# Optimization experiments

Measured on AMD Instinct MI355X. Metric: run time of the kernel, lower is better.

Reference implementation:

```python
import jax, jax.numpy as jnp
import numpy as np


def conv2d(x, w, b):
    # x: [B, Cin, H, W], w: [Cout, Cin, 3, 3] -> SAME 3x3 conv, stride 1
    y = jax.lax.conv_general_dilated(x, w, (1, 1), 'SAME',
                                     dimension_numbers=('NCHW', 'OIHW', 'NCHW'))
    return y + b[None, :, None, None]


def trilinear_interpolation(data, offsets, sample_nums):
    """data: [B, D(frames), C, H, W]; offsets: [B, sample_nums*3, H, W]
    Returns samples [B, sample_nums, C, H, W] via trilinear interp over (d,h,w)."""
    B, D, C, H, W = data.shape
    S = sample_nums
    off = offsets.reshape(B, S, 3, H, W)
    # base 3x3x3 grid centered at middle frame / current pixel
    g = jnp.arange(S)
    kd = (g // 9 - 1).astype(jnp.float32)        # [S]
    kh = ((g // 3) % 3 - 1).astype(jnp.float32)
    kw = (g % 3 - 1).astype(jnp.float32)
    center = (D - 1) / 2.0
    hh = jnp.arange(H, dtype=jnp.float32)
    ww = jnp.arange(W, dtype=jnp.float32)
    pd = center + kd[None, :, None, None] + off[:, :, 0]                 # [B,S,H,W]
    ph = hh[None, None, :, None] + kh[None, :, None, None] + off[:, :, 1]
    pw = ww[None, None, None, :] + kw[None, :, None, None] + off[:, :, 2]
    pd = jnp.clip(pd, 0.0, D - 1.0)
    ph = jnp.clip(ph, 0.0, H - 1.0)
    pw = jnp.clip(pw, 0.0, W - 1.0)
    d0 = jnp.floor(pd); h0 = jnp.floor(ph); w0 = jnp.floor(pw)
    fd = pd - d0; fh = ph - h0; fw = pw - w0
    d0i = d0.astype(jnp.int32); h0i = h0.astype(jnp.int32); w0i = w0.astype(jnp.int32)
    d1i = jnp.minimum(d0i + 1, D - 1)
    h1i = jnp.minimum(h0i + 1, H - 1)
    w1i = jnp.minimum(w0i + 1, W - 1)
    # flatten (d,h,w) for gather, keep channels contiguous
    data_flat = data.transpose(0, 2, 1, 3, 4).reshape(B, C, D * H * W)

    def gather(di, hi, wi):
        idx = ((di * H + hi) * W + wi).reshape(B, 1, S * H * W)
        g_ = jnp.take_along_axis(data_flat, idx, axis=2)   # [B,C,S*H*W]
        return g_.reshape(B, C, S, H, W).transpose(0, 2, 1, 3, 4)  # [B,S,C,H,W]

    out = jnp.zeros((B, S, C, H, W), dtype=data.dtype)
    for di, wd in ((d0i, 1.0 - fd), (d1i, fd)):
        for hi, wh in ((h0i, 1.0 - fh), (h1i, fh)):
            for wi, wwgt in ((w0i, 1.0 - fw), (w1i, fw)):
                wgt = (wd * wh * wwgt)[:, :, None]  # [B,S,1,H,W]
                out = out + wgt * gather(di, hi, wi)
    return out


SAMPLE_NUMS = 27
GROUPS = 3


def setup_inputs() -> dict:
    key = jax.random.key(0)
    ks = jax.random.split(key, 14)
    B, BURST, C, H, W = 4, 5, 3, 256, 256
    in_len = BURST * C          # 15
    ch_w = in_len + 128 + SAMPLE_NUMS * C  # 224
    s = 0.05
    p = lambda k, sh: jax.random.normal(k, sh, dtype=jnp.float32) * s
    return {
        'data': jax.random.normal(ks[0], (B, BURST, C, H, W), dtype=jnp.float32),
        'enc_w1': p(ks[1], (64, in_len, 3, 3)), 'enc_b1': jnp.zeros((64,), jnp.float32),
        'enc_w2': p(ks[2], (128, 64, 3, 3)),    'enc_b2': jnp.zeros((128,), jnp.float32),
        'off_w':  p(ks[3], (SAMPLE_NUMS * 3, 128, 3, 3)), 'off_b': jnp.zeros((SAMPLE_NUMS * 3,), jnp.float32),
        'wc_w1':  p(ks[4], (64, ch_w, 3, 3)),   'wc_b1': jnp.zeros((64,), jnp.float32),
        'wc_w2':  p(ks[5], (64, 64, 3, 3)),     'wc_b2': jnp.zeros((64,), jnp.float32),
        'wc_w3':  p(ks[6], (SAMPLE_NUMS, 64, 3, 3)), 'wc_b3': jnp.zeros((SAMPLE_NUMS,), jnp.float32),
    }


def reference(data, enc_w1, enc_b1, enc_w2, enc_b2, off_w, off_b,
              wc_w1, wc_b1, wc_w2, wc_b2, wc_w3, wc_b3):
    B, D, C, H, W = data.shape
    net_feed = data.reshape(B, D * C, H, W)
    # encoder_decoder proxy: feature [B,128,H,W] + offsets [B,81,H,W]
    f1 = jax.nn.relu(conv2d(net_feed, enc_w1, enc_b1))
    feature = jax.nn.relu(conv2d(f1, enc_w2, enc_b2))
    offsets = conv2d(feature, off_w, off_b)
    samples = trilinear_interpolation(data, offsets, SAMPLE_NUMS)  # [B,S,C,H,W]
    weight_feed = jnp.concatenate([net_feed, feature,
                                   samples.reshape(B, SAMPLE_NUMS * C, H, W)], axis=1)
    h1 = jax.nn.relu(conv2d(weight_feed, wc_w1, wc_b1))
    h2 = jax.nn.relu(conv2d(h1, wc_w2, wc_b2))
    weights = conv2d(h2, wc_w3, wc_b3)  # [B,S,H,W]
    cpg = SAMPLE_NUMS // GROUPS
    s_g = samples.reshape(B, GROUPS, cpg, C, H, W)
    w_g = weights.reshape(B, GROUPS, cpg, H, W)
    # per-group weighted kernel-prediction sum (convolution_3D), scaled by g
    res_i = GROUPS * jnp.einsum('bgkchw,bgkhw->bgchw', s_g, w_g)
    out = jnp.sum(res_i, axis=1) / GROUPS
    return res_i, out, samples
```

## Files before the change

### kernel.cpp

```cpp
#include <hip/hip_runtime.h>


typedef __attribute__((ext_vector_type(8))) short short8;
typedef __attribute__((ext_vector_type(4))) float f32x4;

__device__ __forceinline__ unsigned short f2bf(float f) {
    unsigned int b = __float_as_uint(f);
    b = (b + 0x7fffu + ((b >> 16) & 1u)) >> 16;
    return (unsigned short)b;
}
__device__ __forceinline__ float bf2f(unsigned int u) {
    return __uint_as_float(u << 16);
}
__device__ __forceinline__ unsigned int pack2(float a, float b) {
    return (unsigned int)f2bf(a) | ((unsigned int)f2bf(b) << 16);
}

__global__ __launch_bounds__(256) void prep_kern(
    const float* __restrict__ w1, const float* __restrict__ w2,
    const float* __restrict__ w3, const float* __restrict__ w5,
    const float* __restrict__ w6, const float* __restrict__ w7,
    unsigned short* __restrict__ wpk)
{
    int idx = blockIdx.x * 256 + threadIdx.x;
    if (idx < 460800) {
        const float* w; int off, CinR, CoutR, CoutP, nch, remap;
        if (idx < 18432)       { w = w1; off = 0;      CinR = 15;  CoutR = 64;  CoutP = 64;  nch = 1; remap = 0; }
        else if (idx < 92160)  { w = w2; off = 18432;  CinR = 64;  CoutR = 128; CoutP = 128; nch = 2; remap = 0; }
        else if (idx < 239616) { w = w3; off = 92160;  CinR = 128; CoutR = 81;  CoutP = 128; nch = 4; remap = 0; }
        else if (idx < 387072) { w = w5; off = 239616; CinR = 224; CoutR = 64;  CoutP = 64;  nch = 8; remap = 1; }
        else if (idx < 423936) { w = w6; off = 387072; CinR = 64;  CoutR = 64;  CoutP = 64;  nch = 2; remap = 0; }
        else                   { w = w7; off = 423936; CinR = 64;  CoutR = 27;  CoutP = 64;  nch = 2; remap = 0; }
        int li = idx - off;
        int kin = li & 31;
        int t = li >> 5;
        int co = t % CoutP; t /= CoutP;
        int chunk = t % nch;
        int tap = t / nch;
        int ci = chunk * 32 + kin;
        int cs = -1;
        if (remap) {
            if (ci < 15) cs = ci;
            else if (ci >= 16 && ci <= 224) cs = ci - 1;
        } else {
            if (ci < CinR) cs = ci;
        }
        float val = 0.f;
        if (co < CoutR && cs >= 0)
            val = w[(co * CinR + cs) * 9 + tap];
        wpk[idx] = f2bf(val);
    } else if (idx < 460800 + 8192) {
        wpk[idx] = 0;
    }
}

__global__ __launch_bounds__(256) void convert_data(
    const float* __restrict__ data, unsigned short* __restrict__ concat)
{
    int i = blockIdx.x * 256 + threadIdx.x;
    int b = i >> 16, p = i & 65535;
    int base = i * 232;
#pragma unroll
    for (int c = 0; c < 15; ++c)
        concat[base + c] = f2bf(data[(b * 15 + c) * 65536 + p]);
    concat[base + 15] = 0;
}

__global__ __launch_bounds__(256) void pack_dpk(
    const float* __restrict__ data, unsigned short* __restrict__ dpk)
{
    int i = blockIdx.x * 256 + threadIdx.x;
    int bd = i >> 16, p = i & 65535;
    unsigned int w0 = pack2(data[(bd * 3 + 0) * 65536 + p],
                            data[(bd * 3 + 1) * 65536 + p]);
    unsigned int w1 = (unsigned int)f2bf(data[(bd * 3 + 2) * 65536 + p]);
    *(uint2*)(dpk + i * 4) = make_uint2(w0, w1);
}

__global__ __launch_bounds__(256) void conv_mfma(
    const unsigned short* __restrict__ src, int srcCs, int srcOff,
    const unsigned short* __restrict__ wp, const float* __restrict__ bias,
    int nch, int Cout, int Cout_pad,
    void* __restrict__ dst, int dstCs, int dstOff, int mode, int relu,
    const uint4* __restrict__ zp)
{
    __shared__ uint4 ldsb[2][1584];
    const int tid = threadIdx.x;
    const int lane = tid & 63;
    const int wv = tid >> 6;
    const int bx = blockIdx.x, b = blockIdx.y, bz = blockIdx.z;
    const int x0 = (bx & 3) * 64, y0 = (bx >> 2) * 4;
    const int l15 = lane & 15, l4 = lane >> 4;
    const int mtc = min(4, (Cout - bz * 64 + 15) >> 4);

    f32x4 acc[4][4];
#pragma unroll
    for (int m = 0; m < 4; ++m)
#pragma unroll
        for (int nt = 0; nt < 4; ++nt) acc[m][nt] = (f32x4)0.f;

    auto stage = [&](int buf, int chunk) {
        int ch = srcOff + chunk * 32 + wv * 8;
        bool chok = (ch + 8 <= srcCs);
        const unsigned short* sbase = src + ch;
#pragma unroll
        for (int it = 0; it < 7; ++it) {
            int r = it * 64 + lane;
            if (r < 396) {
                int hy = r / 66, hx = r - hy * 66;
                int y = y0 - 1 + hy, x = x0 - 1 + hx;
                const uint4* g;
                if (chok && (unsigned)y < 256u && (unsigned)x < 256u)
                    g = (const uint4*)(sbase + (b * 65536 + y * 256 + x) * srcCs);
                else
                    g = zp + lane;
                __builtin_amdgcn_global_load_lds(
                    (const __attribute__((address_space(1))) void*)g,
                    (__attribute__((address_space(3))) void*)&ldsb[buf][wv * 396 + it * 64],
                    16, 0, 0);
            }
        }
    };

    stage(0, 0);
    int buf = 0;
    for (int c = 0; c < nch; ++c) {
        __syncthreads();
        if (c + 1 < nch) stage(buf ^ 1, c + 1);
#pragma unroll
        for (int tap = 0; tap < 9; ++tap) {
            const int dy = tap / 3, dx = tap - dy * 3;
            short8 af[4];
#pragma unroll
            for (int m = 0; m < 4; ++m)
                if (m < mtc)
                    af[m] = *(const short8*)(wp +
                        ((tap * nch + c) * Cout_pad + bz * 64 + m * 16 + l15) * 32 + l4 * 8);
#pragma unroll
            for (int nt = 0; nt < 4; ++nt) {
                int hx = nt * 16 + l15 + dx;
                int hy = wv + dy;
                short8 bf = __builtin_bit_cast(short8,
                    ldsb[buf][l4 * 396 + hy * 66 + hx]);
#pragma unroll
                for (int m = 0; m < 4; ++m)
                    if (m < mtc)
                        acc[m][nt] = __builtin_amdgcn_mfma_f32_16x16x32_bf16(
                            af[m], bf, acc[m][nt], 0, 0, 0);
            }
        }
        buf ^= 1;
    }

    const int y = y0 + wv;
#pragma unroll
    for (int m = 0; m < 4; ++m) {
        if (m >= mtc) continue;
        int co0 = bz * 64 + m * 16 + l4 * 4;
#pragma unroll
        for (int nt = 0; nt < 4; ++nt) {
            int x = x0 + nt * 16 + l15;
            float v[4];
#pragma unroll
            for (int e = 0; e < 4; ++e) {
                int co = co0 + e;
                float f = acc[m][nt][e] + ((co < Cout) ? bias[co] : 0.f);
                if (relu) f = fmaxf(f, 0.f);
                v[e] = f;
            }
            if (mode == 0) {
                unsigned short* d = (unsigned short*)dst +
                    ((b * 65536 + y * 256 + x) * dstCs + dstOff + co0);
                if (co0 + 3 < Cout) {
                    uint2 pk = make_uint2(pack2(v[0], v[1]), pack2(v[2], v[3]));
                    *(uint2*)d = pk;
                } else {
#pragma unroll
                    for (int e = 0; e < 4; ++e)
                        if (co0 + e < Cout) d[e] = f2bf(v[e]);
                }
            } else {
                float* d = (float*)dst + (b * dstCs + co0) * 65536 + y * 256 + x;
#pragma unroll
                for (int e = 0; e < 4; ++e)
                    if (co0 + e < Cout) d[e * 65536] = v[e];
            }
        }
    }
}

__global__ __launch_bounds__(256) void conv7_combine(
    const unsigned short* __restrict__ src,
    const unsigned short* __restrict__ wp,
    const float* __restrict__ bias,
    const unsigned short* __restrict__ concat,
    float* __restrict__ res_i, float* __restrict__ outp,
    const uint4* __restrict__ zp)
{
    __shared__ char ldsraw[50688];
    uint4 (*ldsb)[1584] = (uint4(*)[1584])ldsraw;
    float* wlds = (float*)ldsraw;
    const int tid = threadIdx.x;
    const int lane = tid & 63;
    const int wv = tid >> 6;
    const int bx = blockIdx.x, b = blockIdx.y;
    const int x0 = (bx & 3) * 64, y0 = (bx >> 2) * 4;
    const int l15 = lane & 15, l4 = lane >> 4;

    f32x4 acc[2][4];
#pragma unroll
    for (int m = 0; m < 2; ++m)
#pragma unroll
        for (int nt = 0; nt < 4; ++nt) acc[m][nt] = (f32x4)0.f;

    auto stage = [&](int buf, int chunk) {
        int ch = chunk * 32 + wv * 8;
        const unsigned short* sbase = src + ch;
#pragma unroll
        for (int it = 0; it < 7; ++it) {
            int r = it * 64 + lane;
            if (r < 396) {
                int hy = r / 66, hx = r - hy * 66;
                int y = y0 - 1 + hy, x = x0 - 1 + hx;
                const uint4* g;
                if ((unsigned)y < 256u && (unsigned)x < 256u)
                    g = (const uint4*)(sbase + (b * 65536 + y * 256 + x) * 64);
                else
                    g = zp + lane;
                __builtin_amdgcn_global_load_lds(
                    (const __attribute__((address_space(1))) void*)g,
                    (__attribute__((address_space(3))) void*)&ldsb[buf][wv * 396 + it * 64],
                    16, 0, 0);
            }
        }
    };

    stage(0, 0);
    int buf = 0;
    for (int c = 0; c < 2; ++c) {
        __syncthreads();
        if (c + 1 < 2) stage(buf ^ 1, c + 1);
#pragma unroll
        for (int tap = 0; tap < 9; ++tap) {
            const int dy = tap / 3, dx = tap - dy * 3;
            short8 af[2];
#pragma unroll
            for (int m = 0; m < 2; ++m)
                af[m] = *(const short8*)(wp +
                    ((tap * 2 + c) * 64 + m * 16 + l15) * 32 + l4 * 8);
#pragma unroll
            for (int nt = 0; nt < 4; ++nt) {
                int hx = nt * 16 + l15 + dx;
                int hy = wv + dy;
                short8 bf = __builtin_bit_cast(short8,
                    ldsb[buf][l4 * 396 + hy * 66 + hx]);
#pragma unroll
                for (int m = 0; m < 2; ++m)
                    acc[m][nt] = __builtin_amdgcn_mfma_f32_16x16x32_bf16(
                        af[m], bf, acc[m][nt], 0, 0, 0);
            }
        }
        buf ^= 1;
    }

    __syncthreads();
#pragma unroll
    for (int m = 0; m < 2; ++m) {
        int co0 = m * 16 + l4 * 4;
#pragma unroll
        for (int nt = 0; nt < 4; ++nt) {
            int px = nt * 16 + l15;
#pragma unroll
            for (int e = 0; e < 4; ++e) {
                int co = co0 + e;
                wlds[wv * 2112 + px * 33 + co] =
                    acc[m][nt][e] + ((co < 27) ? bias[co] : 0.f);
            }
        }
    }
    __syncthreads();

    const int r = tid >> 6, px = tid & 63;
    const float* wl = wlds + r * 2112 + px * 33;
    const int y = y0 + r, x = x0 + px;
    const int p = y * 256 + x;
    const unsigned short* cp = concat + (b * 65536 + p) * 232 + 144;
    unsigned int sw[41];
    {
        const uint4* gp = (const uint4*)cp;
#pragma unroll
        for (int k = 0; k < 10; ++k) {
            uint4 t = gp[k];
            sw[4 * k] = t.x; sw[4 * k + 1] = t.y;
            sw[4 * k + 2] = t.z; sw[4 * k + 3] = t.w;
        }
        sw[40] = (unsigned int)cp[80];
    }
    float ov[3] = {0.f, 0.f, 0.f};
#pragma unroll
    for (int g = 0; g < 3; ++g) {
        float rr[3] = {0.f, 0.f, 0.f};
#pragma unroll
        for (int k = 0; k < 9; ++k) {
            int s = g * 9 + k;
            float w = wl[s];
            int L0 = 3 * s;
            float s0 = bf2f((sw[L0 >> 1] >> ((L0 & 1) * 16)) & 0xffffu);
            float s1 = bf2f((sw[(L0 + 1) >> 1] >> (((L0 + 1) & 1) * 16)) & 0xffffu);
            float s2 = bf2f((sw[(L0 + 2) >> 1] >> (((L0 + 2) & 1) * 16)) & 0xffffu);
            rr[0] = fmaf(s0, w, rr[0]);
            rr[1] = fmaf(s1, w, rr[1]);
            rr[2] = fmaf(s2, w, rr[2]);
        }
#pragma unroll
        for (int c = 0; c < 3; ++c) {
            res_i[(b * 9 + g * 3 + c) * 65536 + p] = 3.f * rr[c];
            ov[c] += rr[c];
        }
    }
#pragma unroll
    for (int c = 0; c < 3; ++c)
        outp[(b * 3 + c) * 65536 + p] = ov[c];
}

__global__ __launch_bounds__(256) void trilin_kern(
    const unsigned short* __restrict__ dpk, unsigned short* __restrict__ concat,
    float* __restrict__ smp)
{
    int i = blockIdx.x * 256 + threadIdx.x;
    int b = i >> 16, p = i & 65535;
    int y = p >> 8, x = p & 255;
    unsigned short* cptr = concat + i * 232 + 144;

    unsigned int wbuf[41];
    {
        const uint4* gp = (const uint4*)cptr;
#pragma unroll
        for (int k = 0; k < 10; ++k) {
            uint4 t = gp[k];
            wbuf[4 * k] = t.x; wbuf[4 * k + 1] = t.y;
            wbuf[4 * k + 2] = t.z; wbuf[4 * k + 3] = t.w;
        }
        wbuf[40] = (unsigned int)cptr[80];
    }

#pragma unroll
    for (int s = 0; s < 27; ++s) {
        int L0 = 3 * s;
        float o0 = bf2f((wbuf[L0 >> 1] >> ((L0 & 1) * 16)) & 0xffffu);
        float o1 = bf2f((wbuf[(L0 + 1) >> 1] >> (((L0 + 1) & 1) * 16)) & 0xffffu);
        float o2 = bf2f((wbuf[(L0 + 2) >> 1] >> (((L0 + 2) & 1) * 16)) & 0xffffu);

        float kd = (float)(s / 9 - 1);
        float kh = (float)((s / 3) % 3 - 1);
        float kw = (float)(s % 3 - 1);
        float pd = 2.0f + kd + o0;
        float ph = (float)y + kh + o1;
        float pw = (float)x + kw + o2;
        pd = fminf(fmaxf(pd, 0.f), 4.f);
        ph = fminf(fmaxf(ph, 0.f), 255.f);
        pw = fminf(fmaxf(pw, 0.f), 255.f);
        float d0 = floorf(pd), h0 = floorf(ph), w0 = floorf(pw);
        float fd = pd - d0, fh = ph - h0, fw = pw - w0;
        int d0i = (int)d0, h0i = (int)h0, w0i = (int)w0;
        int d1i = min(d0i + 1, 4), h1i = min(h0i + 1, 255), w1i = min(w0i + 1, 255);

        const unsigned short* p0 = dpk + (b * 5 + d0i) * 262144;
        const unsigned short* p1 = dpk + (b * 5 + d1i) * 262144;
        int a00 = ((h0i << 8) + w0i) << 2, a01 = ((h0i << 8) + w1i) << 2;
        int a10 = ((h1i << 8) + w0i) << 2, a11 = ((h1i << 8) + w1i) << 2;
        uint2 q000 = *(const uint2*)(p0 + a00), q001 = *(const uint2*)(p0 + a01);
        uint2 q010 = *(const uint2*)(p0 + a10), q011 = *(const uint2*)(p0 + a11);
        uint2 q100 = *(const uint2*)(p1 + a00), q101 = *(const uint2*)(p1 + a01);
        uint2 q110 = *(const uint2*)(p1 + a10), q111 = *(const uint2*)(p1 + a11);

        float res[3];
#pragma unroll
        for (int c = 0; c < 3; ++c) {
            auto ex = [&](uint2 q) {
                unsigned int u = (c == 0) ? (q.x & 0xffffu)
                              : (c == 1) ? (q.x >> 16) : (q.y & 0xffffu);
                return bf2f(u);
            };
            float r0 = (ex(q000) * (1.f - fw) + ex(q001) * fw) * (1.f - fh)
                     + (ex(q010) * (1.f - fw) + ex(q011) * fw) * fh;
            float r1 = (ex(q100) * (1.f - fw) + ex(q101) * fw) * (1.f - fh)
                     + (ex(q110) * (1.f - fw) + ex(q111) * fw) * fh;
            float r = r0 * (1.f - fd) + r1 * fd;
            res[c] = r;
            smp[((b * 27 + s) * 3 + c) * 65536 + p] = r;
        }
#pragma unroll
        for (int c = 0; c < 3; ++c) {
            int L = L0 + c;
            unsigned int u = (unsigned int)f2bf(res[c]);
            if (L & 1) wbuf[L >> 1] = (wbuf[L >> 1] & 0xffffu) | (u << 16);
            else       wbuf[L >> 1] = (wbuf[L >> 1] & 0xffff0000u) | u;
        }
    }

    wbuf[40] &= 0xffffu;
    uint4* gp = (uint4*)cptr;
#pragma unroll
    for (int k = 0; k < 10; ++k)
        gp[k] = make_uint4(wbuf[4 * k], wbuf[4 * k + 1], wbuf[4 * k + 2], wbuf[4 * k + 3]);
    *(unsigned int*)(cptr + 80) = wbuf[40];
}

extern "C" void kernel_launch(void* const* d_in, const int* in_sizes, int n_in,
                              void* d_out, int out_size, void* d_ws, size_t ws_size,
                              hipStream_t stream)
{
    const float* data   = (const float*)d_in[0];
    const float* enc_w1 = (const float*)d_in[1];
    const float* enc_b1 = (const float*)d_in[2];
    const float* enc_w2 = (const float*)d_in[3];
    const float* enc_b2 = (const float*)d_in[4];
    const float* off_w  = (const float*)d_in[5];
    const float* off_b  = (const float*)d_in[6];
    const float* wc_w1  = (const float*)d_in[7];
    const float* wc_b1  = (const float*)d_in[8];
    const float* wc_w2  = (const float*)d_in[9];
    const float* wc_b2  = (const float*)d_in[10];
    const float* wc_w3  = (const float*)d_in[11];
    const float* wc_b3  = (const float*)d_in[12];

    float* dout  = (float*)d_out;
    float* res_i = dout;
    float* outp  = dout + 2359296;
    float* smp   = dout + 3145728;

    char* ws = (char*)d_ws;
    unsigned short* concat = (unsigned short*)ws;
    unsigned short* buf_a  = (unsigned short*)(ws + 121634816);
    unsigned short* buf_b  = (unsigned short*)(ws + 155189248);
    unsigned short* wpk    = (unsigned short*)(ws + 188743680);
    unsigned short* wp1 = wpk;
    unsigned short* wp2 = wpk + 18432;
    unsigned short* wp3 = wpk + 92160;
    unsigned short* wp5 = wpk + 239616;
    unsigned short* wp6 = wpk + 387072;
    unsigned short* wp7 = wpk + 423936;
    const uint4* zp = (const uint4*)(wpk + 460800);
    unsigned short* dpk = buf_b;

    dim3 blk(256);

    prep_kern<<<1832, blk, 0, stream>>>(enc_w1, enc_w2, off_w, wc_w1, wc_w2, wc_w3, wpk);
    convert_data<<<1024, blk, 0, stream>>>(data, concat);
    pack_dpk<<<5120, blk, 0, stream>>>(data, dpk);

    conv_mfma<<<dim3(256, 4, 1), blk, 0, stream>>>(
        concat, 232, 0, wp1, enc_b1, 1, 64, 64, buf_a, 64, 0, 0, 1, zp);
    conv_mfma<<<dim3(256, 4, 2), blk, 0, stream>>>(
        buf_a, 64, 0, wp2, enc_b2, 2, 128, 128, concat, 232, 16, 0, 1, zp);
    conv_mfma<<<dim3(256, 4, 2), blk, 0, stream>>>(
        concat, 232, 16, wp3, off_b, 4, 81, 128, concat, 232, 144, 0, 0, zp);
    trilin_kern<<<1024, blk, 0, stream>>>(dpk, concat, smp);
    conv_mfma<<<dim3(256, 4, 1), blk, 0, stream>>>(
        concat, 232, 0, wp5, wc_b1, 8, 64, 64, buf_a, 64, 0, 0, 1, zp);
    conv_mfma<<<dim3(256, 4, 1), blk, 0, stream>>>(
        buf_a, 64, 0, wp6, wc_b2, 2, 64, 64, buf_b, 64, 0, 0, 1, zp);
    conv7_combine<<<dim3(256, 4), blk, 0, stream>>>(
        buf_b, wp7, wc_b3, concat, res_i, outp, zp);
}
```

Baseline: 744.2 us.

## Triple-buffer conv staging with explicit vmcnt waits and row-batched weight prefetch

The MFMA conv kernels move from double to triple LDS buffering. Each iteration now prefetches two chunks ahead and uses explicit s_waitcnt vmcnt counts between raw barriers, so global-to-LDS loads overlap compute more deeply. Weight fragments are loaded one filter row ahead of the MFMAs to hide global load latency. Launch bounds request two blocks per SM, and convert_data writes packed 16-byte stores instead of scalar shorts. The trade-off is more LDS and registers per block, and the hand-counted vmcnt must match the number of issued loads.

```diff
diff --git a/kernel.cpp b/kernel.cpp
--- a/kernel.cpp
+++ b/kernel.cpp
@@ -59,11 +59,15 @@
 {
     int i = blockIdx.x * 256 + threadIdx.x;
     int b = i >> 16, p = i & 65535;
-    int base = i * 232;
-#pragma unroll
-    for (int c = 0; c < 15; ++c)
-        concat[base + c] = f2bf(data[(b * 15 + c) * 65536 + p]);
-    concat[base + 15] = 0;
+    unsigned int w[8];
+#pragma unroll
+    for (int k = 0; k < 7; ++k)
+        w[k] = pack2(data[(b * 15 + 2 * k) * 65536 + p],
+                     data[(b * 15 + 2 * k + 1) * 65536 + p]);
+    w[7] = (unsigned int)f2bf(data[(b * 15 + 14) * 65536 + p]);
+    uint4* d = (uint4*)(concat + i * 232);
+    d[0] = make_uint4(w[0], w[1], w[2], w[3]);
+    d[1] = make_uint4(w[4], w[5], w[6], w[7]);
 }
 
 __global__ __launch_bounds__(256) void pack_dpk(
@@ -77,14 +81,14 @@
     *(uint2*)(dpk + i * 4) = make_uint2(w0, w1);
 }
 
-__global__ __launch_bounds__(256) void conv_mfma(
+__global__ __launch_bounds__(256, 2) void conv_mfma(
     const unsigned short* __restrict__ src, int srcCs, int srcOff,
     const unsigned short* __restrict__ wp, const float* __restrict__ bias,
     int nch, int Cout, int Cout_pad,
     void* __restrict__ dst, int dstCs, int dstOff, int mode, int relu,
     const uint4* __restrict__ zp)
 {
-    __shared__ uint4 ldsb[2][1584];
+    __shared__ uint4 ldsb[3 * 1584];
     const int tid = threadIdx.x;
     const int lane = tid & 63;
     const int wv = tid >> 6;
@@ -99,7 +103,8 @@
 #pragma unroll
         for (int nt = 0; nt < 4; ++nt) acc[m][nt] = (f32x4)0.f;
 
-    auto stage = [&](int buf, int chunk) {
+    auto stage = [&](int bufi, int chunk) {
+        uint4* d0 = ldsb + bufi * 1584 + wv * 396;
         int ch = srcOff + chunk * 32 + wv * 8;
         bool chok = (ch + 8 <= srcCs);
         const unsigned short* sbase = src + ch;
@@ -116,40 +121,56 @@
                     g = zp + lane;
                 __builtin_amdgcn_global_load_lds(
                     (const __attribute__((address_space(1))) void*)g,
-                    (__attribute__((address_space(3))) void*)&ldsb[buf][wv * 396 + it * 64],
+                    (__attribute__((address_space(3))) void*)(d0 + it * 64),
                     16, 0, 0);
             }
         }
     };
 
     stage(0, 0);
-    int buf = 0;
+    if (nch > 1) stage(1, 1);
     for (int c = 0; c < nch; ++c) {
-        __syncthreads();
-        if (c + 1 < nch) stage(buf ^ 1, c + 1);
-#pragma unroll
-        for (int tap = 0; tap < 9; ++tap) {
-            const int dy = tap / 3, dx = tap - dy * 3;
-            short8 af[4];
-#pragma unroll
-            for (int m = 0; m < 4; ++m)
-                if (m < mtc)
-                    af[m] = *(const short8*)(wp +
-                        ((tap * nch + c) * Cout_pad + bz * 64 + m * 16 + l15) * 32 + l4 * 8);
-#pragma unroll
-            for (int nt = 0; nt < 4; ++nt) {
-                int hx = nt * 16 + l15 + dx;
-                int hy = wv + dy;
-                short8 bf = __builtin_bit_cast(short8,
-                    ldsb[buf][l4 * 396 + hy * 66 + hx]);
+        __builtin_amdgcn_s_barrier();
+        if (c + 2 < nch) stage((c + 2) % 3, c + 2);
+        if (c + 1 < nch) asm volatile("s_waitcnt vmcnt(7)" ::: "memory");
+        else             asm volatile("s_waitcnt vmcnt(0)" ::: "memory");
+        __builtin_amdgcn_s_barrier();
+
+        const uint4* lb = ldsb + (c % 3) * 1584;
+        short8 A0[3][4], A1[3][4], A2[3][4];
+        auto loadrow = [&](short8 (&A)[3][4], int row) {
+#pragma unroll
+            for (int t = 0; t < 3; ++t)
 #pragma unroll
                 for (int m = 0; m < 4; ++m)
                     if (m < mtc)
-                        acc[m][nt] = __builtin_amdgcn_mfma_f32_16x16x32_bf16(
-                            af[m], bf, acc[m][nt], 0, 0, 0);
-            }
-        }
-        buf ^= 1;
+                        A[t][m] = *(const short8*)(wp +
+                            (((row * 3 + t) * nch + c) * Cout_pad +
+                             bz * 64 + m * 16 + l15) * 32 + l4 * 8);
+        };
+        auto mfmarow = [&](short8 (&A)[3][4], int row) {
+#pragma unroll
+            for (int t = 0; t < 3; ++t) {
+#pragma unroll
+                for (int nt = 0; nt < 4; ++nt) {
+                    int hx = nt * 16 + l15 + t;
+                    int hy = wv + row;
+                    short8 bf = __builtin_bit_cast(short8,
+                        lb[l4 * 396 + hy * 66 + hx]);
+#pragma unroll
+                    for (int m = 0; m < 4; ++m)
+                        if (m < mtc)
+                            acc[m][nt] = __builtin_amdgcn_mfma_f32_16x16x32_bf16(
+                                A[t][m], bf, acc[m][nt], 0, 0, 0);
+                }
+            }
+        };
+        loadrow(A0, 0);
+        loadrow(A1, 1);
+        mfmarow(A0, 0);
+        loadrow(A2, 2);
+        mfmarow(A1, 1);
+        mfmarow(A2, 2);
     }
 
     const int y = y0 + wv;
@@ -189,7 +210,7 @@
     }
 }
 
-__global__ __launch_bounds__(256) void conv7_combine(
+__global__ __launch_bounds__(256, 2) void conv7_combine(
     const unsigned short* __restrict__ src,
     const unsigned short* __restrict__ wp,
     const float* __restrict__ bias,
@@ -197,9 +218,8 @@
     float* __restrict__ res_i, float* __restrict__ outp,
     const uint4* __restrict__ zp)
 {
-    __shared__ char ldsraw[50688];
-    uint4 (*ldsb)[1584] = (uint4(*)[1584])ldsraw;
-    float* wlds = (float*)ldsraw;
+    __shared__ uint4 ldsb[3 * 1584];
+    float* wlds = (float*)ldsb;
     const int tid = threadIdx.x;
     const int lane = tid & 63;
     const int wv = tid >> 6;
@@ -213,7 +233,8 @@
 #pragma unroll
         for (int nt = 0; nt < 4; ++nt) acc[m][nt] = (f32x4)0.f;
 
-    auto stage = [&](int buf, int chunk) {
+    auto stage = [&](int bufi, int chunk) {
+        uint4* d0 = ldsb + bufi * 1584 + wv * 396;
         int ch = chunk * 32 + wv * 8;
         const unsigned short* sbase = src + ch;
 #pragma unroll
@@ -229,38 +250,52 @@
                     g = zp + lane;
                 __builtin_amdgcn_global_load_lds(
                     (const __attribute__((address_space(1))) void*)g,
-                    (__attribute__((address_space(3))) void*)&ldsb[buf][wv * 396 + it * 64],
+                    (__attribute__((address_space(3))) void*)(d0 + it * 64),
                     16, 0, 0);
             }
         }
     };
 
     stage(0, 0);
-    int buf = 0;
+    stage(1, 1);
     for (int c = 0; c < 2; ++c) {
-        __syncthreads();
-        if (c + 1 < 2) stage(buf ^ 1, c + 1);
-#pragma unroll
-        for (int tap = 0; tap < 9; ++tap) {
-            const int dy = tap / 3, dx = tap - dy * 3;
-            short8 af[2];
-#pragma unroll
-            for (int m = 0; m < 2; ++m)
-                af[m] = *(const short8*)(wp +
-                    ((tap * 2 + c) * 64 + m * 16 + l15) * 32 + l4 * 8);
-#pragma unroll
-            for (int nt = 0; nt < 4; ++nt) {
-                int hx = nt * 16 + l15 + dx;
-                int hy = wv + dy;
-                short8 bf = __builtin_bit_cast(short8,
-                    ldsb[buf][l4 * 396 + hy * 66 + hx]);
+        __builtin_amdgcn_s_barrier();
+        if (c + 1 < 2) asm volatile("s_waitcnt vmcnt(7)" ::: "memory");
+        else           asm volatile("s_waitcnt vmcnt(0)" ::: "memory");
+        __builtin_amdgcn_s_barrier();
+
+        const uint4* lb = ldsb + c * 1584;
+        short8 A0[3][2], A1[3][2], A2[3][2];
+        auto loadrow = [&](short8 (&A)[3][2], int row) {
+#pragma unroll
+            for (int t = 0; t < 3; ++t)
 #pragma unroll
                 for (int m = 0; m < 2; ++m)
-                    acc[m][nt] = __builtin_amdgcn_mfma_f32_16x16x32_bf16(
-                        af[m], bf, acc[m][nt], 0, 0, 0);
-            }
-        }
-        buf ^= 1;
+                    A[t][m] = *(const short8*)(wp +
+                        (((row * 3 + t) * 2 + c) * 64 + m * 16 + l15) * 32 + l4 * 8);
+        };
+        auto mfmarow = [&](short8 (&A)[3][2], int row) {
+#pragma unroll
+            for (int t = 0; t < 3; ++t) {
+#pragma unroll
+                for (int nt = 0; nt < 4; ++nt) {
+                    int hx = nt * 16 + l15 + t;
+                    int hy = wv + row;
+                    short8 bf = __builtin_bit_cast(short8,
+                        lb[l4 * 396 + hy * 66 + hx]);
+#pragma unroll
+                    for (int m = 0; m < 2; ++m)
+                        acc[m][nt] = __builtin_amdgcn_mfma_f32_16x16x32_bf16(
+                            A[t][m], bf, acc[m][nt], 0, 0, 0);
+                }
+            }
+        };
+        loadrow(A0, 0);
+        loadrow(A1, 1);
+        mfmarow(A0, 0);
+        loadrow(A2, 2);
+        mfmarow(A1, 1);
+        mfmarow(A2, 2);
     }
 
     __syncthreads();
```

Measured after the change: 973.7 us. 30.8% more time.
